# Kernel optimization log

Hardware: AMD Instinct MI355X
Metric: run time of the kernel (lower is better)

## Reference

```python
import jax, jax.numpy as jnp
import numpy as np

OUT_F, IN_F = 4096, 4096
WEIGHT_NUMEL = OUT_F * IN_F
NUM_CHUNKS, CHUNK_SIZE = 16384, 1024
D_ALPHA, HIDDEN = 64, 256
TOKENS = 256


def setup_inputs() -> dict:
    key = jax.random.key(0)
    ks = jax.random.split(key, 7)
    s = 0.05  # keep activations in a sane range
    return {
        "x": jax.random.normal(ks[0], (TOKENS, IN_F), jnp.float32),
        "codebook": jax.random.normal(ks[1], (NUM_CHUNKS, D_ALPHA), jnp.float32) * s,
        "w1": jax.random.normal(ks[2], (HIDDEN, D_ALPHA), jnp.float32) * s,
        "b1": jax.random.normal(ks[3], (HIDDEN,), jnp.float32) * s,
        "w2": jax.random.normal(ks[4], (CHUNK_SIZE, HIDDEN), jnp.float32) * s,
        "b2": jax.random.normal(ks[5], (CHUNK_SIZE,), jnp.float32) * s,
        "bias": jax.random.normal(ks[6], (OUT_F,), jnp.float32) * s,
    }


def reference(x, codebook, w1, b1, w2, b2, bias):
    # materialize_weight: alpha = codebook[start:start+num_chunks] (here: all rows)
    alpha = codebook[:NUM_CHUNKS]                                  # [num_chunks, d_alpha]
    # shared decoder psi: Linear -> GELU(exact) -> Linear (chunked loop == single GEMM)
    h = jax.nn.gelu(alpha @ w1.T + b1, approximate=False)          # [num_chunks, hidden]
    chunks = h @ w2.T + b2                                         # [num_chunks, chunk_size]
    w = chunks.reshape(-1)[:WEIGHT_NUMEL].reshape(OUT_F, IN_F)     # assemble weight
    # F.linear(x, w, b) = x @ w.T + b
    return x @ w.T + bias
```

## Files before the change

### kernel.cpp

```cpp
#include <hip/hip_runtime.h>
#include <math.h>

#define OUT_F      4096
#define IN_F       4096
#define NUM_CHUNKS 16384
#define CHUNK_SIZE 1024
#define D_ALPHA    64
#define HIDDEN     256
#define TOKENS     256

typedef __attribute__((ext_vector_type(8))) __bf16 bf16x8;
typedef __attribute__((ext_vector_type(4))) __bf16 bf16x4;
typedef __attribute__((ext_vector_type(4))) float f32x4;

__device__ __forceinline__ void gl2lds16(const void* g, void* l) {
    __builtin_amdgcn_global_load_lds(
        (const __attribute__((address_space(1))) void*)g,
        (__attribute__((address_space(3))) void*)l,
        16, 0, 0);
}

__global__ __launch_bounds__(256) void prep_kernel(
    const float* __restrict__ cb, const float* __restrict__ w1,
    const float* __restrict__ b1, const float* __restrict__ x,
    const float* __restrict__ b2, const float* __restrict__ w2,
    __bf16* __restrict__ H, __bf16* __restrict__ Y,
    float* __restrict__ xb2) {
    __shared__ char smem[16384];
    const int b   = blockIdx.x;
    const int tid = threadIdx.x;

    if (b < 1024) {
        const int by = b >> 2;
        const int bx = b & 3;
        const int c0 = by * 64, h0 = bx * 64;
        __bf16* sA = (__bf16*)smem;
        __bf16* sB = (__bf16*)(smem + 8192);
        const float4* cb4 = reinterpret_cast<const float4*>(cb) + (size_t)by * 1024;
        const float4* w14 = reinterpret_cast<const float4*>(w1) + (size_t)bx * 1024;
#pragma unroll
        for (int q = 0; q < 4; ++q) {
            const int idx = q * 256 + tid;
            float4 va = cb4[idx];
            float4 vb = w14[idx];
            bf16x4 oa, ob;
            oa.x = (__bf16)va.x; oa.y = (__bf16)va.y; oa.z = (__bf16)va.z; oa.w = (__bf16)va.w;
            ob.x = (__bf16)vb.x; ob.y = (__bf16)vb.y; ob.z = (__bf16)vb.z; ob.w = (__bf16)vb.w;
            *reinterpret_cast<bf16x4*>(sA + idx * 4) = oa;
            *reinterpret_cast<bf16x4*>(sB + idx * 4) = ob;
        }
        __syncthreads();
        const int wave = tid >> 6, lane = tid & 63;
        const int wm = (wave & 1) * 32, wn = (wave >> 1) * 32;
        const int fr = lane & 15, fq = lane >> 4;
        f32x4 acc[2][2] = {};
        bf16x8 af[2][2], bv[2][2];
#pragma unroll
        for (int i = 0; i < 2; ++i)
#pragma unroll
            for (int u = 0; u < 2; ++u) {
                af[i][u] = *reinterpret_cast<const bf16x8*>(
                    sA + (wm + i * 16 + fr) * 64 + u * 32 + fq * 8);
                bv[i][u] = *reinterpret_cast<const bf16x8*>(
                    sB + (wn + i * 16 + fr) * 64 + u * 32 + fq * 8);
            }
#pragma unroll
        for (int u = 0; u < 2; ++u)
#pragma unroll
            for (int i = 0; i < 2; ++i)
#pragma unroll
                for (int j = 0; j < 2; ++j)
                    acc[i][j] = __builtin_amdgcn_mfma_f32_16x16x32_bf16(
                        af[i][u], bv[j][u], acc[i][j], 0, 0, 0);
#pragma unroll
        for (int j = 0; j < 2; ++j) {
            const int col = h0 + wn + j * 16 + fr;
            const float bb = b1[col];
#pragma unroll
            for (int i = 0; i < 2; ++i) {
                const int rbase = c0 + wm + i * 16 + fq * 4;
#pragma unroll
                for (int r = 0; r < 4; ++r) {
                    float v = acc[i][j][r] + bb;
                    float g = 0.5f * v * (1.0f + erff(v * 0.70710678118654752f));
                    H[(size_t)(rbase + r) * 256 + col] = (__bf16)g;
                }
            }
        }
    } else if (b < 1152) {
        const int yb = b - 1024;
        const int m0 = (yb >> 2) * 32;
        const int n0 = (yb & 3) * 64;
        __bf16* sA = (__bf16*)smem;
        __bf16* sB = (__bf16*)(smem + 32 * 72 * 2);
        const int wave = tid >> 6, lane = tid & 63;
        const int fr = lane & 15, fq = lane >> 4;
        const int wn = wave * 16;
        const float4* xv  = reinterpret_cast<const float4*>(x);
        const float4* w2v = reinterpret_cast<const float4*>(w2);
        f32x4 acc[2] = {};

        for (int k0 = 0; k0 < 1024; k0 += 64) {
#pragma unroll
            for (int q = 0; q < 2; ++q) {
                const int idx = q * 256 + tid;
                const int row = idx >> 4, c = idx & 15;
                float4 v = xv[(size_t)(m0 + row) * 256 + (k0 >> 2) + c];
                bf16x4 o;
                o.x = (__bf16)v.x; o.y = (__bf16)v.y; o.z = (__bf16)v.z; o.w = (__bf16)v.w;
                *reinterpret_cast<bf16x4*>(sA + row * 72 + c * 4) = o;
            }
#pragma unroll
            for (int q = 0; q < 4; ++q) {
                const int idx = q * 256 + tid;
                const int kk = idx >> 4, c = idx & 15;
                float4 v = w2v[(size_t)(k0 + kk) * 64 + (n0 >> 2) + c];
                sB[(c * 4 + 0) * 72 + kk] = (__bf16)v.x;
                sB[(c * 4 + 1) * 72 + kk] = (__bf16)v.y;
                sB[(c * 4 + 2) * 72 + kk] = (__bf16)v.z;
                sB[(c * 4 + 3) * 72 + kk] = (__bf16)v.w;
            }
            __syncthreads();
#pragma unroll
            for (int u = 0; u < 2; ++u) {
                bf16x8 bv = *reinterpret_cast<const bf16x8*>(
                    sB + (wn + fr) * 72 + u * 32 + fq * 8);
#pragma unroll
                for (int i = 0; i < 2; ++i) {
                    bf16x8 af = *reinterpret_cast<const bf16x8*>(
                        sA + (i * 16 + fr) * 72 + u * 32 + fq * 8);
                    acc[i] = __builtin_amdgcn_mfma_f32_16x16x32_bf16(
                        af, bv, acc[i], 0, 0, 0);
                }
            }
            __syncthreads();
        }
#pragma unroll
        for (int i = 0; i < 2; ++i) {
            const int rbase = m0 + i * 16 + fq * 4;
            const int col = n0 + wn + fr;
#pragma unroll
            for (int r = 0; r < 4; ++r)
                Y[(size_t)(rbase + r) * 256 + col] = (__bf16)acc[i][r];
        }
    } else {
        float* ws_ = (float*)smem;
        const int t = b - 1152;
        const float4* xr  = reinterpret_cast<const float4*>(x + (size_t)t * IN_F);
        const float4* b24 = reinterpret_cast<const float4*>(b2);
        float acc = 0.0f;
#pragma unroll
        for (int ii = 0; ii < 4; ++ii) {
            const int idx = ii * 256 + tid;
            float4 v = xr[idx];
            float4 bb = b24[idx & 255];
            acc += v.x * bb.x + v.y * bb.y + v.z * bb.z + v.w * bb.w;
        }
#pragma unroll
        for (int off = 32; off > 0; off >>= 1) acc += __shfl_down(acc, off, 64);
        if ((tid & 63) == 0) ws_[tid >> 6] = acc;
        __syncthreads();
        if (tid == 0) xb2[t] = ws_[0] + ws_[1] + ws_[2] + ws_[3];
    }
}

template <int BK>
__global__ __launch_bounds__(256) void gemm_bt64(
    const __bf16* __restrict__ A, const __bf16* __restrict__ B,
    const float* __restrict__ bias, const float* __restrict__ rowterm,
    float* __restrict__ C, int M, int N, int K) {
    __shared__ __bf16 sA[64 * BK];
    __shared__ __bf16 sB[64 * BK];
    const int tid = threadIdx.x;
    const int m0 = blockIdx.y * 64;
    const int n0 = blockIdx.x * 64;

    constexpr int NC = BK / 32;
    int rowc[NC], colc[NC];
#pragma unroll
    for (int c = 0; c < NC; ++c) {
        const int flat = c * 2048 + tid * 8;
        rowc[c] = flat / BK;
        colc[c] = flat % BK;
    }

    const int wave = tid >> 6, lane = tid & 63;
    const int wm = (wave & 1) * 32, wn = (wave >> 1) * 32;
    const int fr = lane & 15, fq = lane >> 4;

    f32x4 acc[2][2] = {};

    for (int k0 = 0; k0 < K; k0 += BK) {
#pragma unroll
        for (int c = 0; c < NC; ++c) {
            gl2lds16(A + (size_t)(m0 + rowc[c]) * K + k0 + colc[c],
                     sA + c * 2048 + tid * 8);
            gl2lds16(B + (size_t)(n0 + rowc[c]) * K + k0 + colc[c],
                     sB + c * 2048 + tid * 8);
        }
        __syncthreads();

#pragma unroll
        for (int u = 0; u < BK / 32; ++u) {
            bf16x8 af[2], bv[2];
#pragma unroll
            for (int i = 0; i < 2; ++i) {
                af[i] = *reinterpret_cast<const bf16x8*>(
                    sA + (wm + i * 16 + fr) * BK + u * 32 + fq * 8);
                bv[i] = *reinterpret_cast<const bf16x8*>(
                    sB + (wn + i * 16 + fr) * BK + u * 32 + fq * 8);
            }
#pragma unroll
            for (int i = 0; i < 2; ++i)
#pragma unroll
                for (int j = 0; j < 2; ++j)
                    acc[i][j] = __builtin_amdgcn_mfma_f32_16x16x32_bf16(
                        af[i], bv[j], acc[i][j], 0, 0, 0);
        }
        __syncthreads();
    }

#pragma unroll
    for (int j = 0; j < 2; ++j) {
        const int col = n0 + wn + j * 16 + fr;
        const float bvs = bias[col];
#pragma unroll
        for (int i = 0; i < 2; ++i) {
            const int rbase = m0 + wm + i * 16 + fq * 4;
#pragma unroll
            for (int r = 0; r < 4; ++r)
                C[(size_t)(rbase + r) * N + col] =
                    acc[i][j][r] + bvs + rowterm[rbase + r];
        }
    }
}

extern "C" void kernel_launch(void* const* d_in, const int* in_sizes, int n_in,
                              void* d_out, int out_size, void* d_ws, size_t ws_size,
                              hipStream_t stream) {
    const float* x        = (const float*)d_in[0];
    const float* codebook = (const float*)d_in[1];
    const float* w1       = (const float*)d_in[2];
    const float* b1       = (const float*)d_in[3];
    const float* w2       = (const float*)d_in[4];
    const float* b2       = (const float*)d_in[5];
    const float* bias     = (const float*)d_in[6];
    float* out = (float*)d_out;

    char* ws = (char*)d_ws;
    __bf16* H   = (__bf16*)(ws);
    __bf16* Y   = (__bf16*)(ws + (8u << 20));
    float*  xb2 = (float*)(ws + (8u << 20) + (512u << 10));

    prep_kernel<<<1408, 256, 0, stream>>>(codebook, w1, b1, x, b2, w2,
                                          H, Y, xb2);

    {
        dim3 grid(OUT_F / 64, TOKENS / 64, 1);
        gemm_bt64<128><<<grid, 256, 0, stream>>>(
            Y, H, bias, xb2, out, TOKENS, OUT_F, 1024);
    }
}
```

Baseline: 103.7 us.

## Fuse prep and GEMM into one cooperative kernel with grid sync

```diff
diff --git a/kernel.cpp b/kernel.cpp
--- a/kernel.cpp
+++ b/kernel.cpp
@@ -1,5 +1,8 @@
 #include <hip/hip_runtime.h>
+#include <hip/hip_cooperative_groups.h>
 #include <math.h>
+
+namespace cg = cooperative_groups;
 
 #define OUT_F      4096
 #define IN_F       4096
@@ -20,86 +23,89 @@
         16, 0, 0);
 }
 
-__global__ __launch_bounds__(256) void prep_kernel(
+__device__ __forceinline__ float gelu_erf(float v) {
+    return 0.5f * v * (1.0f + erff(v * 0.70710678118654752f));
+}
+
+__global__ __launch_bounds__(256) void fused_kernel(
     const float* __restrict__ cb, const float* __restrict__ w1,
     const float* __restrict__ b1, const float* __restrict__ x,
     const float* __restrict__ b2, const float* __restrict__ w2,
+    const float* __restrict__ bias,
     __bf16* __restrict__ H, __bf16* __restrict__ Y,
-    float* __restrict__ xb2) {
-    __shared__ char smem[16384];
-    const int b   = blockIdx.x;
-    const int tid = threadIdx.x;
-
-    if (b < 1024) {
-        const int by = b >> 2;
-        const int bx = b & 3;
-        const int c0 = by * 64, h0 = bx * 64;
+    float* __restrict__ xb2, float* __restrict__ out)
+{
+    __shared__ __align__(16) char smem[24576];
+    const int b    = blockIdx.x;
+    const int tid  = threadIdx.x;
+    const int wave = tid >> 6, lane = tid & 63;
+    const int fr   = lane & 15, fq = lane >> 4;
+
+    {
         __bf16* sA = (__bf16*)smem;
-        __bf16* sB = (__bf16*)(smem + 8192);
-        const float4* cb4 = reinterpret_cast<const float4*>(cb) + (size_t)by * 1024;
-        const float4* w14 = reinterpret_cast<const float4*>(w1) + (size_t)bx * 1024;
-#pragma unroll
-        for (int q = 0; q < 4; ++q) {
-            const int idx = q * 256 + tid;
-            float4 va = cb4[idx];
-            float4 vb = w14[idx];
-            bf16x4 oa, ob;
-            oa.x = (__bf16)va.x; oa.y = (__bf16)va.y; oa.z = (__bf16)va.z; oa.w = (__bf16)va.w;
-            ob.x = (__bf16)vb.x; ob.y = (__bf16)vb.y; ob.z = (__bf16)vb.z; ob.w = (__bf16)vb.w;
-            *reinterpret_cast<bf16x4*>(sA + idx * 4) = oa;
-            *reinterpret_cast<bf16x4*>(sB + idx * 4) = ob;
-        }
-        __syncthreads();
-        const int wave = tid >> 6, lane = tid & 63;
+        __bf16* sB = (__bf16*)(smem + 9216);
+        const int nt   = (b < 256) ? 1 : 3;
+        const int base = (b < 256) ? b : 256 + (b - 256) * 3;
         const int wm = (wave & 1) * 32, wn = (wave >> 1) * 32;
-        const int fr = lane & 15, fq = lane >> 4;
-        f32x4 acc[2][2] = {};
-        bf16x8 af[2][2], bv[2][2];
-#pragma unroll
-        for (int i = 0; i < 2; ++i)
+        for (int t = 0; t < nt; ++t) {
+            const int tile = base + t;
+            const int by = tile >> 2, bx = tile & 3;
+            const float4* cb4 = reinterpret_cast<const float4*>(cb) + (size_t)by * 1024;
+            const float4* w14 = reinterpret_cast<const float4*>(w1) + (size_t)bx * 1024;
+#pragma unroll
+            for (int q = 0; q < 4; ++q) {
+                const int idx = q * 256 + tid, row = idx >> 4, c = idx & 15;
+                float4 va = cb4[idx], vb = w14[idx];
+                bf16x4 oa, ob;
+                oa.x=(__bf16)va.x; oa.y=(__bf16)va.y; oa.z=(__bf16)va.z; oa.w=(__bf16)va.w;
+                ob.x=(__bf16)vb.x; ob.y=(__bf16)vb.y; ob.z=(__bf16)vb.z; ob.w=(__bf16)vb.w;
+                *reinterpret_cast<bf16x4*>(sA + row * 72 + c * 4) = oa;
+                *reinterpret_cast<bf16x4*>(sB + row * 72 + c * 4) = ob;
+            }
+            __syncthreads();
+            f32x4 acc[2][2] = {};
+            bf16x8 af[2], bv[2];
 #pragma unroll
             for (int u = 0; u < 2; ++u) {
-                af[i][u] = *reinterpret_cast<const bf16x8*>(
-                    sA + (wm + i * 16 + fr) * 64 + u * 32 + fq * 8);
-                bv[i][u] = *reinterpret_cast<const bf16x8*>(
-                    sB + (wn + i * 16 + fr) * 64 + u * 32 + fq * 8);
-            }
-#pragma unroll
-        for (int u = 0; u < 2; ++u)
-#pragma unroll
-            for (int i = 0; i < 2; ++i)
-#pragma unroll
-                for (int j = 0; j < 2; ++j)
-                    acc[i][j] = __builtin_amdgcn_mfma_f32_16x16x32_bf16(
-                        af[i][u], bv[j][u], acc[i][j], 0, 0, 0);
-#pragma unroll
-        for (int j = 0; j < 2; ++j) {
-            const int col = h0 + wn + j * 16 + fr;
-            const float bb = b1[col];
-#pragma unroll
-            for (int i = 0; i < 2; ++i) {
-                const int rbase = c0 + wm + i * 16 + fq * 4;
-#pragma unroll
-                for (int r = 0; r < 4; ++r) {
-                    float v = acc[i][j][r] + bb;
-                    float g = 0.5f * v * (1.0f + erff(v * 0.70710678118654752f));
-                    H[(size_t)(rbase + r) * 256 + col] = (__bf16)g;
+#pragma unroll
+                for (int i = 0; i < 2; ++i) {
+                    af[i] = *reinterpret_cast<const bf16x8*>(
+                        sA + (wm + i * 16 + fr) * 72 + u * 32 + fq * 8);
+                    bv[i] = *reinterpret_cast<const bf16x8*>(
+                        sB + (wn + i * 16 + fr) * 72 + u * 32 + fq * 8);
                 }
-            }
-        }
-    } else if (b < 1152) {
-        const int yb = b - 1024;
-        const int m0 = (yb >> 2) * 32;
-        const int n0 = (yb & 3) * 64;
+#pragma unroll
+                for (int i = 0; i < 2; ++i)
+#pragma unroll
+                    for (int j = 0; j < 2; ++j)
+                        acc[i][j] = __builtin_amdgcn_mfma_f32_16x16x32_bf16(
+                            af[i], bv[j], acc[i][j], 0, 0, 0);
+            }
+#pragma unroll
+            for (int j = 0; j < 2; ++j) {
+                const int col = bx * 64 + wn + j * 16 + fr;
+                const float bb = b1[col];
+#pragma unroll
+                for (int i = 0; i < 2; ++i) {
+                    const int rbase = by * 64 + wm + i * 16 + fq * 4;
+#pragma unroll
+                    for (int r = 0; r < 4; ++r)
+                        H[(size_t)(rbase + r) * 256 + col] =
+                            (__bf16)gelu_erf(acc[i][j][r] + bb);
+                }
+            }
+            __syncthreads();
+        }
+    }
+
+    if (b < 256) {
         __bf16* sA = (__bf16*)smem;
-        __bf16* sB = (__bf16*)(smem + 32 * 72 * 2);
-        const int wave = tid >> 6, lane = tid & 63;
-        const int fr = lane & 15, fq = lane >> 4;
-        const int wn = wave * 16;
+        __bf16* sB = (__bf16*)(smem + 4608);
+        const int m0 = (b >> 3) * 32, n0 = (b & 7) * 32;
+        const int wm = (wave & 1) * 16, wn = (wave >> 1) * 16;
         const float4* xv  = reinterpret_cast<const float4*>(x);
         const float4* w2v = reinterpret_cast<const float4*>(w2);
-        f32x4 acc[2] = {};
-
+        f32x4 acc = {};
         for (int k0 = 0; k0 < 1024; k0 += 64) {
 #pragma unroll
             for (int q = 0; q < 2; ++q) {
@@ -107,13 +113,13 @@
                 const int row = idx >> 4, c = idx & 15;
                 float4 v = xv[(size_t)(m0 + row) * 256 + (k0 >> 2) + c];
                 bf16x4 o;
-                o.x = (__bf16)v.x; o.y = (__bf16)v.y; o.z = (__bf16)v.z; o.w = (__bf16)v.w;
+                o.x=(__bf16)v.x; o.y=(__bf16)v.y; o.z=(__bf16)v.z; o.w=(__bf16)v.w;
                 *reinterpret_cast<bf16x4*>(sA + row * 72 + c * 4) = o;
             }
 #pragma unroll
-            for (int q = 0; q < 4; ++q) {
+            for (int q = 0; q < 2; ++q) {
                 const int idx = q * 256 + tid;
-                const int kk = idx >> 4, c = idx & 15;
+                const int kk = idx >> 3, c = idx & 7;
                 float4 v = w2v[(size_t)(k0 + kk) * 64 + (n0 >> 2) + c];
                 sB[(c * 4 + 0) * 72 + kk] = (__bf16)v.x;
                 sB[(c * 4 + 1) * 72 + kk] = (__bf16)v.y;
@@ -123,29 +129,20 @@
             __syncthreads();
 #pragma unroll
             for (int u = 0; u < 2; ++u) {
+                bf16x8 af = *reinterpret_cast<const bf16x8*>(
+                    sA + (wm + fr) * 72 + u * 32 + fq * 8);
                 bf16x8 bv = *reinterpret_cast<const bf16x8*>(
                     sB + (wn + fr) * 72 + u * 32 + fq * 8);
-#pragma unroll
-                for (int i = 0; i < 2; ++i) {
-                    bf16x8 af = *reinterpret_cast<const bf16x8*>(
-                        sA + (i * 16 + fr) * 72 + u * 32 + fq * 8);
-                    acc[i] = __builtin_amdgcn_mfma_f32_16x16x32_bf16(
-                        af, bv, acc[i], 0, 0, 0);
-                }
-            }
-            __syncthreads();
-        }
-#pragma unroll
-        for (int i = 0; i < 2; ++i) {
-            const int rbase = m0 + i * 16 + fq * 4;
-            const int col = n0 + wn + fr;
-#pragma unroll
-            for (int r = 0; r < 4; ++r)
-                Y[(size_t)(rbase + r) * 256 + col] = (__bf16)acc[i][r];
-        }
+                acc = __builtin_amdgcn_mfma_f32_16x16x32_bf16(af, bv, acc, 0, 0, 0);
+            }
+            __syncthreads();
+        }
+#pragma unroll
+        for (int r = 0; r < 4; ++r)
+            Y[(size_t)(m0 + wm + fq * 4 + r) * 256 + n0 + wn + fr] = (__bf16)acc[r];
     } else {
         float* ws_ = (float*)smem;
-        const int t = b - 1152;
+        const int t = b - 256;
         const float4* xr  = reinterpret_cast<const float4*>(x + (size_t)t * IN_F);
         const float4* b24 = reinterpret_cast<const float4*>(b2);
         float acc = 0.0f;
@@ -161,76 +158,58 @@
         if ((tid & 63) == 0) ws_[tid >> 6] = acc;
         __syncthreads();
         if (tid == 0) xb2[t] = ws_[0] + ws_[1] + ws_[2] + ws_[3];
-    }
-}
-
-template <int BK>
-__global__ __launch_bounds__(256) void gemm_bt64(
-    const __bf16* __restrict__ A, const __bf16* __restrict__ B,
-    const float* __restrict__ bias, const float* __restrict__ rowterm,
-    float* __restrict__ C, int M, int N, int K) {
-    __shared__ __bf16 sA[64 * BK];
-    __shared__ __bf16 sB[64 * BK];
-    const int tid = threadIdx.x;
-    const int m0 = blockIdx.y * 64;
-    const int n0 = blockIdx.x * 64;
-
-    constexpr int NC = BK / 32;
-    int rowc[NC], colc[NC];
-#pragma unroll
-    for (int c = 0; c < NC; ++c) {
-        const int flat = c * 2048 + tid * 8;
-        rowc[c] = flat / BK;
-        colc[c] = flat % BK;
-    }
-
-    const int wave = tid >> 6, lane = tid & 63;
-    const int wm = (wave & 1) * 32, wn = (wave >> 1) * 32;
-    const int fr = lane & 15, fq = lane >> 4;
-
-    f32x4 acc[2][2] = {};
-
-    for (int k0 = 0; k0 < K; k0 += BK) {
-#pragma unroll
-        for (int c = 0; c < NC; ++c) {
-            gl2lds16(A + (size_t)(m0 + rowc[c]) * K + k0 + colc[c],
-                     sA + c * 2048 + tid * 8);
-            gl2lds16(B + (size_t)(n0 + rowc[c]) * K + k0 + colc[c],
-                     sB + c * 2048 + tid * 8);
-        }
-        __syncthreads();
-
-#pragma unroll
-        for (int u = 0; u < BK / 32; ++u) {
-            bf16x8 af[2], bv[2];
-#pragma unroll
-            for (int i = 0; i < 2; ++i) {
-                af[i] = *reinterpret_cast<const bf16x8*>(
-                    sA + (wm + i * 16 + fr) * BK + u * 32 + fq * 8);
-                bv[i] = *reinterpret_cast<const bf16x8*>(
-                    sB + (wn + i * 16 + fr) * BK + u * 32 + fq * 8);
-            }
-#pragma unroll
-            for (int i = 0; i < 2; ++i)
-#pragma unroll
-                for (int j = 0; j < 2; ++j)
-                    acc[i][j] = __builtin_amdgcn_mfma_f32_16x16x32_bf16(
-                        af[i], bv[j], acc[i][j], 0, 0, 0);
-        }
         __syncthreads();
     }
 
-#pragma unroll
-    for (int j = 0; j < 2; ++j) {
-        const int col = n0 + wn + j * 16 + fr;
-        const float bvs = bias[col];
-#pragma unroll
-        for (int i = 0; i < 2; ++i) {
-            const int rbase = m0 + wm + i * 16 + fq * 4;
+    cg::this_grid().sync();
+
+    {
+        __bf16* sA2 = (__bf16*)smem;
+        __bf16* sB2 = (__bf16*)(smem + 8192);
+        const __bf16* A = Y;
+        const __bf16* B = H;
+        const int m0 = (b >> 6) * 32;
+        const int n0 = (b & 63) * 64;
+        const int wm = (wave & 1) * 16;
+        const int wn = (wave >> 1) * 32;
+        f32x4 acc[2] = {};
+        for (int k0 = 0; k0 < 1024; k0 += 128) {
+#pragma unroll
+            for (int cc = 0; cc < 2; ++cc) {
+                const int flat = cc * 2048 + tid * 8;
+                gl2lds16(A + (size_t)(m0 + (flat >> 7)) * 1024 + k0 + (flat & 127),
+                         sA2 + flat);
+            }
+#pragma unroll
+            for (int cc = 0; cc < 4; ++cc) {
+                const int flat = cc * 2048 + tid * 8;
+                gl2lds16(B + (size_t)(n0 + (flat >> 7)) * 1024 + k0 + (flat & 127),
+                         sB2 + flat);
+            }
+            __syncthreads();
+#pragma unroll
+            for (int u = 0; u < 4; ++u) {
+                bf16x8 af = *reinterpret_cast<const bf16x8*>(
+                    sA2 + (wm + fr) * 128 + u * 32 + fq * 8);
+#pragma unroll
+                for (int j = 0; j < 2; ++j) {
+                    bf16x8 bv = *reinterpret_cast<const bf16x8*>(
+                        sB2 + (wn + j * 16 + fr) * 128 + u * 32 + fq * 8);
+                    acc[j] = __builtin_amdgcn_mfma_f32_16x16x32_bf16(
+                        af, bv, acc[j], 0, 0, 0);
+                }
+            }
+            __syncthreads();
+        }
+#pragma unroll
+        for (int j = 0; j < 2; ++j) {
+            const int col = n0 + wn + j * 16 + fr;
+            const float bvs = bias[col];
+            const int rbase = m0 + wm + fq * 4;
 #pragma unroll
             for (int r = 0; r < 4; ++r)
-                C[(size_t)(rbase + r) * N + col] =
-                    acc[i][j][r] + bvs + rowterm[rbase + r];
+                out[(size_t)(rbase + r) * 4096 + col] =
+                    acc[j][r] + bvs + xb2[rbase + r];
         }
     }
 }
@@ -252,12 +231,9 @@
     __bf16* Y   = (__bf16*)(ws + (8u << 20));
     float*  xb2 = (float*)(ws + (8u << 20) + (512u << 10));
 
-    prep_kernel<<<1408, 256, 0, stream>>>(codebook, w1, b1, x, b2, w2,
-                                          H, Y, xb2);
-
-    {
-        dim3 grid(OUT_F / 64, TOKENS / 64, 1);
-        gemm_bt64<128><<<grid, 256, 0, stream>>>(
-            Y, H, bias, xb2, out, TOKENS, OUT_F, 1024);
-    }
-}
+    void* kargs[] = {(void*)&codebook, (void*)&w1, (void*)&b1, (void*)&x,
+                     (void*)&b2, (void*)&w2, (void*)&bias,
+                     (void*)&H, (void*)&Y, (void*)&xb2, (void*)&out};
+    hipLaunchCooperativeKernel(fused_kernel, dim3(512), dim3(256),
+                               kargs, 0, stream);
+}
```

Result: slower. 177.8 us (+71.4%).

## Shrink GEMM M-tile to 32 and XOR-swizzle LDS to avoid bank conflicts

Applied to the files above, without the earlier changes.

```diff
diff --git a/kernel.cpp b/kernel.cpp
--- a/kernel.cpp
+++ b/kernel.cpp
@@ -164,58 +164,50 @@
     }
 }
 
-template <int BK>
-__global__ __launch_bounds__(256) void gemm_bt64(
+__global__ __launch_bounds__(256) void gemm_out(
     const __bf16* __restrict__ A, const __bf16* __restrict__ B,
     const float* __restrict__ bias, const float* __restrict__ rowterm,
-    float* __restrict__ C, int M, int N, int K) {
-    __shared__ __bf16 sA[64 * BK];
-    __shared__ __bf16 sB[64 * BK];
+    float* __restrict__ C) {
+    __shared__ __bf16 sA[32 * 128];
+    __shared__ __bf16 sB[64 * 128];
     const int tid = threadIdx.x;
-    const int m0 = blockIdx.y * 64;
+    const int m0 = blockIdx.y * 32;
     const int n0 = blockIdx.x * 64;
-
-    constexpr int NC = BK / 32;
-    int rowc[NC], colc[NC];
-#pragma unroll
-    for (int c = 0; c < NC; ++c) {
-        const int flat = c * 2048 + tid * 8;
-        rowc[c] = flat / BK;
-        colc[c] = flat % BK;
-    }
-
     const int wave = tid >> 6, lane = tid & 63;
-    const int wm = (wave & 1) * 32, wn = (wave >> 1) * 32;
+    const int wm = (wave & 1) * 16, wn = (wave >> 1) * 32;
     const int fr = lane & 15, fq = lane >> 4;
-
-    f32x4 acc[2][2] = {};
-
-    for (int k0 = 0; k0 < K; k0 += BK) {
-#pragma unroll
-        for (int c = 0; c < NC; ++c) {
-            gl2lds16(A + (size_t)(m0 + rowc[c]) * K + k0 + colc[c],
-                     sA + c * 2048 + tid * 8);
-            gl2lds16(B + (size_t)(n0 + rowc[c]) * K + k0 + colc[c],
-                     sB + c * 2048 + tid * 8);
-        }
-        __syncthreads();
-
-#pragma unroll
-        for (int u = 0; u < BK / 32; ++u) {
-            bf16x8 af[2], bv[2];
-#pragma unroll
-            for (int i = 0; i < 2; ++i) {
-                af[i] = *reinterpret_cast<const bf16x8*>(
-                    sA + (wm + i * 16 + fr) * BK + u * 32 + fq * 8);
-                bv[i] = *reinterpret_cast<const bf16x8*>(
-                    sB + (wn + i * 16 + fr) * BK + u * 32 + fq * 8);
-            }
-#pragma unroll
-            for (int i = 0; i < 2; ++i)
-#pragma unroll
-                for (int j = 0; j < 2; ++j)
-                    acc[i][j] = __builtin_amdgcn_mfma_f32_16x16x32_bf16(
-                        af[i], bv[j], acc[i][j], 0, 0, 0);
+    const int sw = (fr & 7) << 3;
+
+    f32x4 acc[2] = {};
+
+    for (int k0 = 0; k0 < 1024; k0 += 128) {
+#pragma unroll
+        for (int cc = 0; cc < 2; ++cc) {
+            const int flat = cc * 2048 + tid * 8;
+            const int row = flat >> 7, col = flat & 127;
+            gl2lds16(A + (size_t)(m0 + row) * 1024 + k0 + (col ^ ((row & 7) << 3)),
+                     sA + flat);
+        }
+#pragma unroll
+        for (int cc = 0; cc < 4; ++cc) {
+            const int flat = cc * 2048 + tid * 8;
+            const int row = flat >> 7, col = flat & 127;
+            gl2lds16(B + (size_t)(n0 + row) * 1024 + k0 + (col ^ ((row & 7) << 3)),
+                     sB + flat);
+        }
+        __syncthreads();
+
+#pragma unroll
+        for (int u = 0; u < 4; ++u) {
+            bf16x8 af = *reinterpret_cast<const bf16x8*>(
+                sA + (wm + fr) * 128 + ((u * 32 + fq * 8) ^ sw));
+#pragma unroll
+            for (int j = 0; j < 2; ++j) {
+                bf16x8 bv = *reinterpret_cast<const bf16x8*>(
+                    sB + (wn + j * 16 + fr) * 128 + ((u * 32 + fq * 8) ^ sw));
+                acc[j] = __builtin_amdgcn_mfma_f32_16x16x32_bf16(
+                    af, bv, acc[j], 0, 0, 0);
+            }
         }
         __syncthreads();
     }
@@ -224,14 +216,11 @@
     for (int j = 0; j < 2; ++j) {
         const int col = n0 + wn + j * 16 + fr;
         const float bvs = bias[col];
-#pragma unroll
-        for (int i = 0; i < 2; ++i) {
-            const int rbase = m0 + wm + i * 16 + fq * 4;
-#pragma unroll
-            for (int r = 0; r < 4; ++r)
-                C[(size_t)(rbase + r) * N + col] =
-                    acc[i][j][r] + bvs + rowterm[rbase + r];
-        }
+        const int rbase = m0 + wm + fq * 4;
+#pragma unroll
+        for (int r = 0; r < 4; ++r)
+            C[(size_t)(rbase + r) * 4096 + col] =
+                acc[j][r] + bvs + rowterm[rbase + r];
     }
 }
 
@@ -256,8 +245,7 @@
                                           H, Y, xb2);
 
     {
-        dim3 grid(OUT_F / 64, TOKENS / 64, 1);
-        gemm_bt64<128><<<grid, 256, 0, stream>>>(
-            Y, H, bias, xb2, out, TOKENS, OUT_F, 1024);
-    }
-}
+        dim3 grid(OUT_F / 64, TOKENS / 32, 1);
+        gemm_out<<<grid, 256, 0, stream>>>(Y, H, bias, xb2, out);
+    }
+}
```

Measured after the change: 97.51 us. 6.0% less time.
